# Optimization experiments

Hardware: AMD Instinct MI355X
Metric: run time of the kernel (lower is better)

## Reference

```python
import jax, jax.numpy as jnp
import numpy as np

B, D_IN, M, D_MEM = 65536, 64, 2048, 64


def setup_inputs() -> dict:
    key = jax.random.key(0)
    k = jax.random.split(key, 5)
    glorot = lambda kk, shape: jax.random.uniform(
        kk, shape, jnp.float32,
        -jnp.sqrt(6.0 / (shape[0] + shape[1])), jnp.sqrt(6.0 / (shape[0] + shape[1])))
    return {
        "inputs": jax.random.normal(k[0], (B, D_IN), jnp.float32),
        "W_att": glorot(k[1], (D_IN, M)),
        "b_att": jnp.zeros((M,), jnp.float32),
        "W_write": glorot(k[2], (D_IN, D_MEM)),
        "b_write": jnp.zeros((D_MEM,), jnp.float32),
        "memory": glorot(k[3], (M, D_MEM)),
        "update_gate": jnp.full((M,), 0.5, jnp.float32),
    }


def reference(inputs, W_att, b_att, W_write, b_write, memory, update_gate):
    # Read attention: Dense(memory_size, softmax) -> [B, M]
    read_attention = jax.nn.softmax(inputs @ W_att + b_att, axis=-1)
    # Read: [B, M] @ [M, Dm] -> [B, Dm]
    read_vector = read_attention @ memory
    # Write candidate: Dense(memory_dim, tanh) -> [B, Dm]
    candidate_write = jnp.tanh(inputs @ W_write + b_write)
    aggregated_write = jnp.mean(candidate_write, axis=0)[None, :]  # [1, Dm]
    write_attention = jnp.mean(read_attention, axis=0)             # [M]
    update_weights = (write_attention * update_gate)[:, None]      # [M, 1]
    # Gated in-place memory update (returned as new state)
    new_memory = memory * (1.0 - update_weights) + update_weights * aggregated_write
    return read_vector, new_memory
```

## Files before the change

### kernel.cpp

```cpp
#include <hip/hip_runtime.h>
#include <hip/hip_bf16.h>

typedef unsigned int   u32;
typedef unsigned short u16;

typedef __bf16 bf16x8 __attribute__((ext_vector_type(8)));
typedef float  f32x4  __attribute__((ext_vector_type(4)));
typedef u32    u32x4  __attribute__((ext_vector_type(4)));
typedef u32    u32x2  __attribute__((ext_vector_type(2)));

union Frag { u32x4 u; bf16x8 b; };

#define MFMA16 __builtin_amdgcn_mfma_f32_16x16x32_bf16

#define B_ROWS 65536
#define D_IN   64
#define M_SZ   2048
#define D_MEM  64

#define WT_OFF      0
#define MEMT_OFF    262144
#define WWT_OFF     524288
#define CSF_OFF     532480
#define AGF_OFF     540672
#define BATTS_OFF   540928

#define L2E 1.4426950408889634f

#define AS1 __attribute__((address_space(1)))
#define AS3 __attribute__((address_space(3)))

#if defined(__has_builtin)
#if __has_builtin(__builtin_amdgcn_global_load_lds)
#define HAS_GLD 1
#endif
#endif
#ifndef HAS_GLD
#define HAS_GLD 0
#endif

__device__ __forceinline__ float bf2f(u16 h) { return __uint_as_float(((u32)h) << 16); }
__device__ __forceinline__ u16 f2bf(float f) {
    u32 u = __float_as_uint(f);
    return (u16)((u + 0x7FFFu + ((u >> 16) & 1u)) >> 16);
}
#if defined(__has_builtin) && __has_builtin(__builtin_amdgcn_exp2f)
__device__ __forceinline__ float exp2fast(float x) { return __builtin_amdgcn_exp2f(x); }
#else
__device__ __forceinline__ float exp2fast(float x) { return __expf(x * 0.6931471805599453f); }
#endif
__device__ __forceinline__ float tanh_fast(float x) {
    const float e = exp2fast(x * (2.0f * L2E));
    return 1.0f - 2.0f * __builtin_amdgcn_rcpf(e + 1.0f);
}
__device__ __forceinline__ bool detect_bf16(const void* ug) {
    return ((const u32*)ug)[0] == 0x3F003F00u;
}
__device__ __forceinline__ float load_elem(const void* p, size_t i, bool isbf) {
    return isbf ? bf2f(((const u16*)p)[i]) : ((const float*)p)[i];
}

__device__ __forceinline__ u32 cvtpk_bf16(float lo, float hi) {
    u32 r;
    asm("v_cvt_pk_bf16_f32 %0, %1, %2" : "=v"(r) : "v"(lo), "v"(hi));
    return r;
}
#if defined(__has_builtin) && __has_builtin(__builtin_amdgcn_permlane32_swap) && \
    __has_builtin(__builtin_amdgcn_permlane16_swap)
__device__ __forceinline__ void pl32swap(u32& a, u32& b) {
    u32x2 r = __builtin_amdgcn_permlane32_swap(a, b, false, false);
    a = r[0]; b = r[1];
}
__device__ __forceinline__ void pl16swap(u32& a, u32& b) {
    u32x2 r = __builtin_amdgcn_permlane16_swap(a, b, false, false);
    a = r[0]; b = r[1];
}
#else
__device__ __forceinline__ void pl32swap(u32& a, u32& b) {
    asm("v_permlane32_swap_b32 %0, %1" : "+v"(a), "+v"(b));
}
__device__ __forceinline__ void pl16swap(u32& a, u32& b) {
    asm("v_permlane16_swap_b32 %0, %1" : "+v"(a), "+v"(b));
}
#endif
template<int CTRL>
__device__ __forceinline__ float xadd(float v) {
    int x = __builtin_amdgcn_update_dpp(0, __float_as_int(v), CTRL, 0xF, 0xF, true);
    return v + __int_as_float(x);
}

__global__ void __launch_bounds__(256)
prep_kernel(const void* Watt, const void* mem_in, const void* Wwr,
            const void* batt_in, const void* ug,
            u16* Wt, u16* memT, u16* Wwt, float* CSF, float* battS)
{
    const bool isbf = detect_bf16(ug);
    const int b = blockIdx.x;
    const int t = threadIdx.x;
    if (b == 65) {
        for (int i = t; i < 2112; i += 256) CSF[i] = 0.f;
        for (int i = t; i < 2048; i += 256)
            battS[i] = load_elem(batt_in, i, isbf) * L2E;
        return;
    }
    __shared__ u16 tile[64][65];
    const void* src; u16* dst; int C, rb, cb, bsel;
    if (b < 32)      { src = Watt;   dst = Wt;   C = 2048; rb = 0;           cb = b * 64; bsel = 0; }
    else if (b < 64) { src = mem_in; dst = memT; C = 64;   rb = (b-32) * 64; cb = 0;      bsel = 1; }
    else             { src = Wwr;    dst = Wwt;  C = 64;   rb = 0;           cb = 0;      bsel = 2; }

#pragma unroll
    for (int j = 0; j < 16; ++j) {
        int e = j * 256 + t;
        int r = e >> 6, c = e & 63;
        float v = load_elem(src, (size_t)(rb + r) * C + cb + c, isbf);
        tile[r][c] = f2bf(v);
    }
    __syncthreads();

#pragma unroll
    for (int it = 0; it < 2; ++it) {
        const int task = it * 256 + t;
        const int row = task >> 3, blk = task & 7;
        u32x4 w;
        u16* wp = (u16*)&w;
#pragma unroll
        for (int i = 0; i < 8; ++i) wp[i] = tile[blk * 8 + i][row];
        if (bsel == 0) {
            const int m = cb + row;
            const int kb = (blk ^ m) & 7;
            *(u32x4*)&dst[(size_t)m * 64 + kb * 8] = w;
        } else if (bsel == 1) {
            const int mb = (blk ^ row) & 7;
            *(u32x4*)&dst[(size_t)row * 2048 + rb + mb * 8] = w;
        } else {
            *(u32x4*)&dst[(size_t)row * 64 + blk * 8] = w;
        }
    }
}

__global__ void __launch_bounds__(256, 2)
main_kernel(const void* x_in, const void* bwrite_in,
            const u16* __restrict__ Wt, const u16* __restrict__ memT,
            const u16* __restrict__ Wwt, const float* __restrict__ battS,
            const void* ug, float* CSF, float* AGF, void* out)
{
    const bool isbf = detect_bf16(ug);
    const int tid = threadIdx.x;
    const int lane = tid & 63, wave = tid >> 6;
    const int quad = lane >> 4, l4 = lane & 15;
    const int rowbase = blockIdx.x * 128;

    __shared__ __align__(16) u16 WtA[2][8192];
    __shared__ __align__(16) u16 MeL[2][64][128];
    __shared__ float csA[2112];

    const int wvu = __builtin_amdgcn_readfirstlane(wave);

    for (int i = tid; i < 2112; i += 256) csA[i] = 0.f;

    auto cp16 = [&](const char* gsrc_lane, char* lds_base_uniform) {
#if HAS_GLD
        __builtin_amdgcn_global_load_lds((const AS1 void*)gsrc_lane,
                                         (AS3 void*)lds_base_uniform, 16, 0, 0);
#else
        *(u32x4*)(lds_base_uniform + lane * 16) = *(const u32x4*)gsrc_lane;
#endif
    };
    auto stageWt = [&](int ch, int b) {
        char* lb = (char*)&WtA[b][0] + wvu * 4096;
        const char* gb = (const char*)Wt + (size_t)ch * 16384 + wvu * 4096 + lane * 16;
#pragma unroll
        for (int j = 0; j < 4; ++j)
            cp16(gb + j * 1024, lb + j * 1024);
    };
    auto stageMe = [&](int ch, int b) {
        char* lb = (char*)&MeL[b][0][0] + wvu * 4096;
        const char* gb = (const char*)memT + (size_t)(wvu * 16 + (lane >> 4)) * 4096
                       + (size_t)ch * 256 + (lane & 15) * 16;
#pragma unroll
        for (int j = 0; j < 4; ++j)
            cp16(gb + (size_t)j * 16384, lb + j * 1024);
    };

    Frag a[2][2];
#pragma unroll
    for (int rg = 0; rg < 2; ++rg) {
        const int arow = rowbase + wave * 32 + rg * 16 + l4;
        if (isbf) {
            const u16* xp = (const u16*)x_in + (size_t)arow * 64 + quad * 8;
            a[rg][0].u = *(const u32x4*)xp;
            a[rg][1].u = *(const u32x4*)(xp + 32);
        } else {
            const float* xp = (const float*)x_in + (size_t)arow * 64 + quad * 8;
#pragma unroll
            for (int j = 0; j < 8; ++j) {
                ((u16*)&a[rg][0])[j] = f2bf(xp[j]);
                ((u16*)&a[rg][1])[j] = f2bf(xp[32 + j]);
            }
        }
    }
    const f32x4 zf = {0.f, 0.f, 0.f, 0.f};

    stageWt(0, 0);

    float agout = 0.f;
    {
#pragma unroll
        for (int t = 0; t < 4; ++t) {
            const u16* bp = Wwt + (size_t)(t * 16 + l4) * 64 + quad * 8;
            Frag b0, b1; b0.u = *(const u32x4*)bp; b1.u = *(const u32x4*)(bp + 32);
            const float bw = load_elem(bwrite_in, t * 16 + l4, isbf);
            float s = 0.f;
#pragma unroll
            for (int rg = 0; rg < 2; ++rg) {
                f32x4 acc = MFMA16(a[rg][0].b, b0.b, zf, 0, 0, 0);
                acc = MFMA16(a[rg][1].b, b1.b, acc, 0, 0, 0);
#pragma unroll
                for (int i = 0; i < 4; ++i) s += tanh_fast(acc[i] + bw);
            }
            s += __shfl_xor(s, 16, 64);
            s += __shfl_xor(s, 32, 64);
            if (quad == t) agout = s;
        }
    }

    __syncthreads();
    atomicAdd(&csA[2048 + lane], agout);

    float lsum[2] = {0.f, 0.f};
    auto p1body = [&](int ch, int buf) {
#pragma unroll
        for (int half = 0; half < 2; ++half) {
            const int mb = half * 64;
            const int mbase = ch * 128 + mb;
            Frag wb0[4], wb1[4]; f32x4 blv[4];
#pragma unroll
            for (int t = 0; t < 4; ++t) {
                const int rr = mb + t * 16 + l4, swr = rr & 7;
                wb0[t].u = *(const u32x4*)&WtA[buf][rr * 64 + ((quad ^ swr) << 3)];
                wb1[t].u = *(const u32x4*)&WtA[buf][rr * 64 + (((quad + 4) ^ swr) << 3)];
                blv[t] = *(const f32x4*)&battS[mbase + t * 16 + quad * 4];
            }
#pragma unroll
            for (int rg = 0; rg < 2; ++rg)
#pragma unroll
                for (int t = 0; t < 4; ++t) {
                    f32x4 acc = MFMA16(wb0[t].b, a[rg][0].b, zf, 0, 0, 0);
                    acc = MFMA16(wb1[t].b, a[rg][1].b, acc, 0, 0, 0);
#pragma unroll
                    for (int i = 0; i < 4; ++i)
                        lsum[rg] += exp2fast(fmaf(acc[i], L2E, blv[t][i]));
                }
        }
    };
    for (int chp = 0; chp < 8; ++chp) {
        const int ch0 = 2 * chp, ch1 = ch0 + 1;
        stageWt(ch1, 1);
        p1body(ch0, 0);
        __syncthreads();
        if (ch1 < 15) stageWt(ch1 + 1, 0);
        p1body(ch1, 1);
        __syncthreads();
    }
    float invl[2];
#pragma unroll
    for (int rg = 0; rg < 2; ++rg) {
        float v = lsum[rg];
        v += __shfl_xor(v, 16, 64);
        v += __shfl_xor(v, 32, 64);
        invl[rg] = 1.f / v;
    }

    f32x4 oaccT[2][4] = {{zf,zf,zf,zf},{zf,zf,zf,zf}};
    stageMe(15, 1);
    __syncthreads();
    const bool sb0 = (l4 & 1), sb1 = (l4 & 2), sb2 = (l4 & 4), sb3 = (l4 & 8);
    auto p2body = [&](int ch, int buf) {
#pragma unroll
        for (int half = 0; half < 2; ++half) {
            const int mb = half * 64;
            const int mbase = ch * 128 + mb;
            const int mbh8 = mb >> 3;
            Frag wb0[4], wb1[4], mb0[4], mb1[4]; f32x4 blv[4];
#pragma unroll
            for (int t = 0; t < 4; ++t) {
                const int rr = mb + t * 16 + l4, swr = rr & 7;
                wb0[t].u = *(const u32x4*)&WtA[buf][rr * 64 + ((quad ^ swr) << 3)];
                wb1[t].u = *(const u32x4*)&WtA[buf][rr * 64 + (((quad + 4) ^ swr) << 3)];
                const int dd = t * 16 + l4, swd = dd & 7;
                mb0[t].u = *(const u32x4*)&MeL[buf][dd][(mbh8 | (quad ^ swd)) << 3];
                mb1[t].u = *(const u32x4*)&MeL[buf][dd][(mbh8 | ((quad + 4) ^ swd)) << 3];
                blv[t] = *(const f32x4*)&battS[mbase + t * 16 + quad * 4];
            }
            float c16[16];
#pragma unroll
            for (int j = 0; j < 16; ++j) c16[j] = 0.f;
#pragma unroll
            for (int rg = 0; rg < 2; ++rg) {
                u32 P0[4], P1[4];
                const float il = invl[rg];
#pragma unroll
                for (int t = 0; t < 4; ++t) {
                    f32x4 acc = MFMA16(wb0[t].b, a[rg][0].b, zf, 0, 0, 0);
                    acc = MFMA16(wb1[t].b, a[rg][1].b, acc, 0, 0, 0);
                    const float e0 = exp2fast(fmaf(acc[0], L2E, blv[t][0]));
                    const float e1 = exp2fast(fmaf(acc[1], L2E, blv[t][1]));
                    const float e2 = exp2fast(fmaf(acc[2], L2E, blv[t][2]));
                    const float e3 = exp2fast(fmaf(acc[3], L2E, blv[t][3]));
                    c16[t * 4 + 0] = fmaf(e0, il, c16[t * 4 + 0]);
                    c16[t * 4 + 1] = fmaf(e1, il, c16[t * 4 + 1]);
                    c16[t * 4 + 2] = fmaf(e2, il, c16[t * 4 + 2]);
                    c16[t * 4 + 3] = fmaf(e3, il, c16[t * 4 + 3]);
                    P0[t] = cvtpk_bf16(e0, e1);
                    P1[t] = cvtpk_bf16(e2, e3);
                }
#pragma unroll
                for (int cc2 = 0; cc2 < 2; ++cc2) {
                    u32 b0 = P0[2 * cc2], b2 = P0[2 * cc2 + 1];
                    u32 b1 = P1[2 * cc2], b3 = P1[2 * cc2 + 1];
                    pl32swap(b0, b2); pl16swap(b0, b2);
                    pl32swap(b1, b3); pl16swap(b1, b3);
                    Frag bf; bf.u = (u32x4){b0, b1, b2, b3};
#pragma unroll
                    for (int dt = 0; dt < 4; ++dt) {
                        if (cc2 == 0)
                            oaccT[rg][dt] = MFMA16(mb0[dt].b, bf.b, oaccT[rg][dt], 0, 0, 0);
                        else
                            oaccT[rg][dt] = MFMA16(mb1[dt].b, bf.b, oaccT[rg][dt], 0, 0, 0);
                    }
                }
            }
            float u8[8];
#pragma unroll
            for (int k = 0; k < 8; ++k) {
                const float t0 = xadd<0xB1>(c16[2 * k]);
                const float t1 = xadd<0xB1>(c16[2 * k + 1]);
                u8[k] = sb0 ? t1 : t0;
            }
            float v4[4];
#pragma unroll
            for (int k = 0; k < 4; ++k) {
                const float t0 = xadd<0x4E>(u8[2 * k]);
                const float t1 = xadd<0x4E>(u8[2 * k + 1]);
                v4[k] = sb1 ? t1 : t0;
            }
            float w2[2];
#pragma unroll
            for (int k = 0; k < 2; ++k) {
                const float t0 = xadd<0x128>(v4[2 * k]);
                const float t1 = xadd<0x128>(v4[2 * k + 1]);
                w2[k] = sb3 ? t1 : t0;
            }
            const float f0 = w2[0] + __shfl_xor(w2[0], 4, 64);
            const float f1 = w2[1] + __shfl_xor(w2[1], 4, 64);
            const float csv = sb2 ? f1 : f0;
            const int tsel = ((l4 >> 3) & 1) | (((l4 >> 2) & 1) << 1);
            const int mout = mbase + tsel * 16 + quad * 4 + (l4 & 3);
            atomicAdd(&csA[mout], csv);
        }
    };
    for (int chp = 7; chp >= 0; --chp) {
        const int ch1 = 2 * chp + 1, ch0 = ch1 - 1;
        stageWt(ch0, 0); stageMe(ch0, 0);
        p2body(ch1, 1);
        __syncthreads();
        if (ch0 > 0) { stageWt(ch0 - 1, 1); stageMe(ch0 - 1, 1); }
        p2body(ch0, 0);
        __syncthreads();
    }

    for (int i = tid; i < 2048; i += 256) atomicAdd(&CSF[i], csA[i]);
    if (tid < 64) atomicAdd(&AGF[tid], csA[2048 + tid]);

#pragma unroll
    for (int rg = 0; rg < 2; ++rg)
#pragma unroll
        for (int dt = 0; dt < 4; ++dt) {
            const int gr = rowbase + wave * 32 + rg * 16 + l4;
            const int d0 = dt * 16 + quad * 4;
            const f32x4 o = oaccT[rg][dt] * invl[rg];
            if (isbf) {
                u32x2 w;
                w.x = cvtpk_bf16(o[0], o[1]);
                w.y = cvtpk_bf16(o[2], o[3]);
                *(u32x2*)&((u16*)out)[(size_t)gr * 64 + d0] = w;
            } else {
                *(f32x4*)&((float*)out)[(size_t)gr * 64 + d0] = o;
            }
        }
}

__global__ void __launch_bounds__(256)
finalize_kernel(const void* mem_in, const void* ug,
                const float* __restrict__ CSF, const float* __restrict__ AGF,
                void* out)
{
    const bool isbf = detect_bf16(ug);
    const int gid = blockIdx.x * 256 + threadIdx.x;
    const int base = gid * 4;
    const int m = base >> 6, d0 = base & 63;
    const float wa  = CSF[m] * (1.f / 65536.f);
    const float uw  = wa * load_elem(ug, m, isbf);
    float o[4];
#pragma unroll
    for (int j = 0; j < 4; ++j) {
        const float agg = AGF[d0 + j] * (1.f / 65536.f);
        const float mv  = load_elem(mem_in, (size_t)base + j, isbf);
        o[j] = mv * (1.f - uw) + uw * agg;
    }
    if (isbf) {
        u32x2 w;
        w.x = cvtpk_bf16(o[0], o[1]);
        w.y = cvtpk_bf16(o[2], o[3]);
        *(u32x2*)&((u16*)out)[(size_t)4194304 + base] = w;
    } else {
        f32x4 w = {o[0], o[1], o[2], o[3]};
        *(f32x4*)&((float*)out)[(size_t)4194304 + base] = w;
    }
}

extern "C" void kernel_launch(void* const* d_in, const int* in_sizes, int n_in,
                              void* d_out, int out_size, void* d_ws, size_t ws_size,
                              hipStream_t stream)
{
    (void)in_sizes; (void)n_in; (void)out_size; (void)ws_size;
    const void* x    = d_in[0];
    const void* Watt = d_in[1];
    const void* batt = d_in[2];
    const void* Wwr  = d_in[3];
    const void* bwr  = d_in[4];
    const void* mem  = d_in[5];
    const void* ug   = d_in[6];

    char* ws = (char*)d_ws;
    u16*   Wt    = (u16*)(ws + WT_OFF);
    u16*   memT  = (u16*)(ws + MEMT_OFF);
    u16*   Wwt   = (u16*)(ws + WWT_OFF);
    float* CSF   = (float*)(ws + CSF_OFF);
    float* AGF   = (float*)(ws + AGF_OFF);
    float* battS = (float*)(ws + BATTS_OFF);

    prep_kernel<<<66, 256, 0, stream>>>(Watt, mem, Wwr, batt, ug,
                                        Wt, memT, Wwt, CSF, battS);
    main_kernel<<<512, 256, 0, stream>>>(x, bwr, Wt, memT, Wwt, battS, ug,
                                         CSF, AGF, d_out);
    finalize_kernel<<<128, 256, 0, stream>>>(mem, ug, CSF, AGF, d_out);
}
```

Baseline: 177.5 us.

## Read weight and memory fragments directly from global memory instead of LDS staging

Removes the double-buffered LDS staging of W_att and memory tiles (global_load_lds plus block barriers) and has each wave load its MFMA fragments straight from global memory, relying on L2/L1 caching. The XOR swizzle in the transpose prep kernel is dropped to match the unswizzled direct reads, and the launch bounds target is raised from 2 to 4 blocks per CU since LDS use drops sharply. Barriers inside the loops go away, but every wave now refetches the same weight data from cache and global load latency is no longer hidden by explicit prefetching.

```diff
diff --git a/kernel.cpp b/kernel.cpp
--- a/kernel.cpp
+++ b/kernel.cpp
@@ -26,18 +26,6 @@
 #define BATTS_OFF   540928
 
 #define L2E 1.4426950408889634f
-
-#define AS1 __attribute__((address_space(1)))
-#define AS3 __attribute__((address_space(3)))
-
-#if defined(__has_builtin)
-#if __has_builtin(__builtin_amdgcn_global_load_lds)
-#define HAS_GLD 1
-#endif
-#endif
-#ifndef HAS_GLD
-#define HAS_GLD 0
-#endif
 
 __device__ __forceinline__ float bf2f(u16 h) { return __uint_as_float(((u32)h) << 16); }
 __device__ __forceinline__ u16 f2bf(float f) {
@@ -127,19 +115,16 @@
 #pragma unroll
         for (int i = 0; i < 8; ++i) wp[i] = tile[blk * 8 + i][row];
         if (bsel == 0) {
-            const int m = cb + row;
-            const int kb = (blk ^ m) & 7;
-            *(u32x4*)&dst[(size_t)m * 64 + kb * 8] = w;
+            *(u32x4*)&dst[(size_t)(cb + row) * 64 + blk * 8] = w;
         } else if (bsel == 1) {
-            const int mb = (blk ^ row) & 7;
-            *(u32x4*)&dst[(size_t)row * 2048 + rb + mb * 8] = w;
+            *(u32x4*)&dst[(size_t)row * 2048 + rb + blk * 8] = w;
         } else {
             *(u32x4*)&dst[(size_t)row * 64 + blk * 8] = w;
         }
     }
 }
 
-__global__ void __launch_bounds__(256, 2)
+__global__ void __launch_bounds__(256, 4)
 main_kernel(const void* x_in, const void* bwrite_in,
             const u16* __restrict__ Wt, const u16* __restrict__ memT,
             const u16* __restrict__ Wwt, const float* __restrict__ battS,
@@ -151,37 +136,9 @@
     const int quad = lane >> 4, l4 = lane & 15;
     const int rowbase = blockIdx.x * 128;
 
-    __shared__ __align__(16) u16 WtA[2][8192];
-    __shared__ __align__(16) u16 MeL[2][64][128];
     __shared__ float csA[2112];
 
-    const int wvu = __builtin_amdgcn_readfirstlane(wave);
-
     for (int i = tid; i < 2112; i += 256) csA[i] = 0.f;
-
-    auto cp16 = [&](const char* gsrc_lane, char* lds_base_uniform) {
-#if HAS_GLD
-        __builtin_amdgcn_global_load_lds((const AS1 void*)gsrc_lane,
-                                         (AS3 void*)lds_base_uniform, 16, 0, 0);
-#else
-        *(u32x4*)(lds_base_uniform + lane * 16) = *(const u32x4*)gsrc_lane;
-#endif
-    };
-    auto stageWt = [&](int ch, int b) {
-        char* lb = (char*)&WtA[b][0] + wvu * 4096;
-        const char* gb = (const char*)Wt + (size_t)ch * 16384 + wvu * 4096 + lane * 16;
-#pragma unroll
-        for (int j = 0; j < 4; ++j)
-            cp16(gb + j * 1024, lb + j * 1024);
-    };
-    auto stageMe = [&](int ch, int b) {
-        char* lb = (char*)&MeL[b][0][0] + wvu * 4096;
-        const char* gb = (const char*)memT + (size_t)(wvu * 16 + (lane >> 4)) * 4096
-                       + (size_t)ch * 256 + (lane & 15) * 16;
-#pragma unroll
-        for (int j = 0; j < 4; ++j)
-            cp16(gb + (size_t)j * 16384, lb + j * 1024);
-    };
 
     Frag a[2][2];
 #pragma unroll
@@ -202,8 +159,6 @@
     }
     const f32x4 zf = {0.f, 0.f, 0.f, 0.f};
 
-    stageWt(0, 0);
-
     float agout = 0.f;
     {
 #pragma unroll
@@ -224,44 +179,33 @@
             if (quad == t) agout = s;
         }
     }
-
     __syncthreads();
     atomicAdd(&csA[2048 + lane], agout);
 
+    const u16* wt_l = Wt + (size_t)(l4)*64 + quad * 8;
+    const u16* me_l = memT + (size_t)(l4)*2048 + quad * 8;
+
     float lsum[2] = {0.f, 0.f};
-    auto p1body = [&](int ch, int buf) {
-#pragma unroll
-        for (int half = 0; half < 2; ++half) {
-            const int mb = half * 64;
-            const int mbase = ch * 128 + mb;
-            Frag wb0[4], wb1[4]; f32x4 blv[4];
+    for (int c = 0; c < 32; ++c) {
+        const int mbase = c * 64;
+        Frag wb0[4], wb1[4]; f32x4 blv[4];
+#pragma unroll
+        for (int t = 0; t < 4; ++t) {
+            const u16* wp = wt_l + (size_t)(mbase + t * 16) * 64;
+            wb0[t].u = *(const u32x4*)wp;
+            wb1[t].u = *(const u32x4*)(wp + 32);
+            blv[t] = *(const f32x4*)&battS[mbase + t * 16 + quad * 4];
+        }
+#pragma unroll
+        for (int rg = 0; rg < 2; ++rg)
 #pragma unroll
             for (int t = 0; t < 4; ++t) {
-                const int rr = mb + t * 16 + l4, swr = rr & 7;
-                wb0[t].u = *(const u32x4*)&WtA[buf][rr * 64 + ((quad ^ swr) << 3)];
-                wb1[t].u = *(const u32x4*)&WtA[buf][rr * 64 + (((quad + 4) ^ swr) << 3)];
-                blv[t] = *(const f32x4*)&battS[mbase + t * 16 + quad * 4];
-            }
-#pragma unroll
-            for (int rg = 0; rg < 2; ++rg)
-#pragma unroll
-                for (int t = 0; t < 4; ++t) {
-                    f32x4 acc = MFMA16(wb0[t].b, a[rg][0].b, zf, 0, 0, 0);
-                    acc = MFMA16(wb1[t].b, a[rg][1].b, acc, 0, 0, 0);
-#pragma unroll
-                    for (int i = 0; i < 4; ++i)
-                        lsum[rg] += exp2fast(fmaf(acc[i], L2E, blv[t][i]));
-                }
-        }
-    };
-    for (int chp = 0; chp < 8; ++chp) {
-        const int ch0 = 2 * chp, ch1 = ch0 + 1;
-        stageWt(ch1, 1);
-        p1body(ch0, 0);
-        __syncthreads();
-        if (ch1 < 15) stageWt(ch1 + 1, 0);
-        p1body(ch1, 1);
-        __syncthreads();
+                f32x4 acc = MFMA16(wb0[t].b, a[rg][0].b, zf, 0, 0, 0);
+                acc = MFMA16(wb1[t].b, a[rg][1].b, acc, 0, 0, 0);
+#pragma unroll
+                for (int i = 0; i < 4; ++i)
+                    lsum[rg] += exp2fast(fmaf(acc[i], L2E, blv[t][i]));
+            }
     }
     float invl[2];
 #pragma unroll
@@ -273,103 +217,88 @@
     }
 
     f32x4 oaccT[2][4] = {{zf,zf,zf,zf},{zf,zf,zf,zf}};
-    stageMe(15, 1);
+    const bool sb0 = (l4 & 1), sb1 = (l4 & 2), sb2 = (l4 & 4), sb3 = (l4 & 8);
+    for (int c = 0; c < 32; ++c) {
+        const int mbase = c * 64;
+        Frag wb0[4], wb1[4], mb0[4], mb1[4]; f32x4 blv[4];
+#pragma unroll
+        for (int t = 0; t < 4; ++t) {
+            const u16* wp = wt_l + (size_t)(mbase + t * 16) * 64;
+            wb0[t].u = *(const u32x4*)wp;
+            wb1[t].u = *(const u32x4*)(wp + 32);
+            const u16* mp = me_l + (size_t)(t * 16) * 2048 + mbase;
+            mb0[t].u = *(const u32x4*)mp;
+            mb1[t].u = *(const u32x4*)(mp + 32);
+            blv[t] = *(const f32x4*)&battS[mbase + t * 16 + quad * 4];
+        }
+        float c16[16];
+#pragma unroll
+        for (int j = 0; j < 16; ++j) c16[j] = 0.f;
+#pragma unroll
+        for (int rg = 0; rg < 2; ++rg) {
+            u32 P0[4], P1[4];
+            const float il = invl[rg];
+#pragma unroll
+            for (int t = 0; t < 4; ++t) {
+                f32x4 acc = MFMA16(wb0[t].b, a[rg][0].b, zf, 0, 0, 0);
+                acc = MFMA16(wb1[t].b, a[rg][1].b, acc, 0, 0, 0);
+                const float e0 = exp2fast(fmaf(acc[0], L2E, blv[t][0]));
+                const float e1 = exp2fast(fmaf(acc[1], L2E, blv[t][1]));
+                const float e2 = exp2fast(fmaf(acc[2], L2E, blv[t][2]));
+                const float e3 = exp2fast(fmaf(acc[3], L2E, blv[t][3]));
+                c16[t * 4 + 0] = fmaf(e0, il, c16[t * 4 + 0]);
+                c16[t * 4 + 1] = fmaf(e1, il, c16[t * 4 + 1]);
+                c16[t * 4 + 2] = fmaf(e2, il, c16[t * 4 + 2]);
+                c16[t * 4 + 3] = fmaf(e3, il, c16[t * 4 + 3]);
+                P0[t] = cvtpk_bf16(e0, e1);
+                P1[t] = cvtpk_bf16(e2, e3);
+            }
+#pragma unroll
+            for (int cc2 = 0; cc2 < 2; ++cc2) {
+                u32 b0 = P0[2 * cc2], b2 = P0[2 * cc2 + 1];
+                u32 b1 = P1[2 * cc2], b3 = P1[2 * cc2 + 1];
+                pl32swap(b0, b2); pl16swap(b0, b2);
+                pl32swap(b1, b3); pl16swap(b1, b3);
+                Frag bf; bf.u = (u32x4){b0, b1, b2, b3};
+#pragma unroll
+                for (int dt = 0; dt < 4; ++dt) {
+                    if (cc2 == 0)
+                        oaccT[rg][dt] = MFMA16(mb0[dt].b, bf.b, oaccT[rg][dt], 0, 0, 0);
+                    else
+                        oaccT[rg][dt] = MFMA16(mb1[dt].b, bf.b, oaccT[rg][dt], 0, 0, 0);
+                }
+            }
+        }
+        float u8[8];
+#pragma unroll
+        for (int k = 0; k < 8; ++k) {
+            const float t0 = xadd<0xB1>(c16[2 * k]);
+            const float t1 = xadd<0xB1>(c16[2 * k + 1]);
+            u8[k] = sb0 ? t1 : t0;
+        }
+        float v4[4];
+#pragma unroll
+        for (int k = 0; k < 4; ++k) {
+            const float t0 = xadd<0x4E>(u8[2 * k]);
+            const float t1 = xadd<0x4E>(u8[2 * k + 1]);
+            v4[k] = sb1 ? t1 : t0;
+        }
+        float w2[2];
+#pragma unroll
+        for (int k = 0; k < 2; ++k) {
+            const float t0 = xadd<0x128>(v4[2 * k]);
+            const float t1 = xadd<0x128>(v4[2 * k + 1]);
+            w2[k] = sb3 ? t1 : t0;
+        }
+        const float f0 = w2[0] + __shfl_xor(w2[0], 4, 64);
+        const float f1 = w2[1] + __shfl_xor(w2[1], 4, 64);
+        const float csv = sb2 ? f1 : f0;
+        const int tsel = ((l4 >> 3) & 1) | (((l4 >> 2) & 1) << 1);
+        const int mout = mbase + tsel * 16 + quad * 4 + (l4 & 3);
+        atomicAdd(&csA[mout], csv);
+    }
+
     __syncthreads();
-    const bool sb0 = (l4 & 1), sb1 = (l4 & 2), sb2 = (l4 & 4), sb3 = (l4 & 8);
-    auto p2body = [&](int ch, int buf) {
-#pragma unroll
-        for (int half = 0; half < 2; ++half) {
-            const int mb = half * 64;
-            const int mbase = ch * 128 + mb;
-            const int mbh8 = mb >> 3;
-            Frag wb0[4], wb1[4], mb0[4], mb1[4]; f32x4 blv[4];
-#pragma unroll
-            for (int t = 0; t < 4; ++t) {
-                const int rr = mb + t * 16 + l4, swr = rr & 7;
-                wb0[t].u = *(const u32x4*)&WtA[buf][rr * 64 + ((quad ^ swr) << 3)];
-                wb1[t].u = *(const u32x4*)&WtA[buf][rr * 64 + (((quad + 4) ^ swr) << 3)];
-                const int dd = t * 16 + l4, swd = dd & 7;
-                mb0[t].u = *(const u32x4*)&MeL[buf][dd][(mbh8 | (quad ^ swd)) << 3];
-                mb1[t].u = *(const u32x4*)&MeL[buf][dd][(mbh8 | ((quad + 4) ^ swd)) << 3];
-                blv[t] = *(const f32x4*)&battS[mbase + t * 16 + quad * 4];
-            }
-            float c16[16];
-#pragma unroll
-            for (int j = 0; j < 16; ++j) c16[j] = 0.f;
-#pragma unroll
-            for (int rg = 0; rg < 2; ++rg) {
-                u32 P0[4], P1[4];
-                const float il = invl[rg];
-#pragma unroll
-                for (int t = 0; t < 4; ++t) {
-                    f32x4 acc = MFMA16(wb0[t].b, a[rg][0].b, zf, 0, 0, 0);
-                    acc = MFMA16(wb1[t].b, a[rg][1].b, acc, 0, 0, 0);
-                    const float e0 = exp2fast(fmaf(acc[0], L2E, blv[t][0]));
-                    const float e1 = exp2fast(fmaf(acc[1], L2E, blv[t][1]));
-                    const float e2 = exp2fast(fmaf(acc[2], L2E, blv[t][2]));
-                    const float e3 = exp2fast(fmaf(acc[3], L2E, blv[t][3]));
-                    c16[t * 4 + 0] = fmaf(e0, il, c16[t * 4 + 0]);
-                    c16[t * 4 + 1] = fmaf(e1, il, c16[t * 4 + 1]);
-                    c16[t * 4 + 2] = fmaf(e2, il, c16[t * 4 + 2]);
-                    c16[t * 4 + 3] = fmaf(e3, il, c16[t * 4 + 3]);
-                    P0[t] = cvtpk_bf16(e0, e1);
-                    P1[t] = cvtpk_bf16(e2, e3);
-                }
-#pragma unroll
-                for (int cc2 = 0; cc2 < 2; ++cc2) {
-                    u32 b0 = P0[2 * cc2], b2 = P0[2 * cc2 + 1];
-                    u32 b1 = P1[2 * cc2], b3 = P1[2 * cc2 + 1];
-                    pl32swap(b0, b2); pl16swap(b0, b2);
-                    pl32swap(b1, b3); pl16swap(b1, b3);
-                    Frag bf; bf.u = (u32x4){b0, b1, b2, b3};
-#pragma unroll
-                    for (int dt = 0; dt < 4; ++dt) {
-                        if (cc2 == 0)
-                            oaccT[rg][dt] = MFMA16(mb0[dt].b, bf.b, oaccT[rg][dt], 0, 0, 0);
-                        else
-                            oaccT[rg][dt] = MFMA16(mb1[dt].b, bf.b, oaccT[rg][dt], 0, 0, 0);
-                    }
-                }
-            }
-            float u8[8];
-#pragma unroll
-            for (int k = 0; k < 8; ++k) {
-                const float t0 = xadd<0xB1>(c16[2 * k]);
-                const float t1 = xadd<0xB1>(c16[2 * k + 1]);
-                u8[k] = sb0 ? t1 : t0;
-            }
-            float v4[4];
-#pragma unroll
-            for (int k = 0; k < 4; ++k) {
-                const float t0 = xadd<0x4E>(u8[2 * k]);
-                const float t1 = xadd<0x4E>(u8[2 * k + 1]);
-                v4[k] = sb1 ? t1 : t0;
-            }
-            float w2[2];
-#pragma unroll
-            for (int k = 0; k < 2; ++k) {
-                const float t0 = xadd<0x128>(v4[2 * k]);
-                const float t1 = xadd<0x128>(v4[2 * k + 1]);
-                w2[k] = sb3 ? t1 : t0;
-            }
-            const float f0 = w2[0] + __shfl_xor(w2[0], 4, 64);
-            const float f1 = w2[1] + __shfl_xor(w2[1], 4, 64);
-            const float csv = sb2 ? f1 : f0;
-            const int tsel = ((l4 >> 3) & 1) | (((l4 >> 2) & 1) << 1);
-            const int mout = mbase + tsel * 16 + quad * 4 + (l4 & 3);
-            atomicAdd(&csA[mout], csv);
-        }
-    };
-    for (int chp = 7; chp >= 0; --chp) {
-        const int ch1 = 2 * chp + 1, ch0 = ch1 - 1;
-        stageWt(ch0, 0); stageMe(ch0, 0);
-        p2body(ch1, 1);
-        __syncthreads();
-        if (ch0 > 0) { stageWt(ch0 - 1, 1); stageMe(ch0 - 1, 1); }
-        p2body(ch0, 0);
-        __syncthreads();
-    }
-
     for (int i = tid; i < 2048; i += 256) atomicAdd(&CSF[i], csA[i]);
     if (tid < 64) atomicAdd(&AGF[tid], csA[2048 + tid]);
 
```

After: 287.1 us. +61.7%, slower.
